# Optimization experiments

Hardware: AMD Instinct MI355X
Metric: run time of the kernel (lower is better)

The kernel has to match this reference:

```python
import jax, jax.numpy as jnp
import numpy as np

NX = 2048
NL = 20
BATCH = 512
EIGMAX = 10.0
EPS = 1e-9


def prox_cardan(eta, x):
    """Prox of u -> -eta*(log(u)+log(1-u)) at x: unique root in (0,1) of
    u^3 - (1+x)u^2 + (x-2eta)u + eta = 0 (Cardano / trigonometric method)."""
    b = -(1.0 + x)
    c = x - 2.0 * eta
    d = eta
    p = c - b * b / 3.0
    q = 2.0 * b ** 3 / 27.0 - b * c / 3.0 + d
    disc = -4.0 * p ** 3 - 27.0 * q ** 2
    # three-real-roots branch (trigonometric); requires p<0
    pm = jnp.minimum(p, -1e-12)
    m = 2.0 * jnp.sqrt(-pm / 3.0)
    arg = jnp.clip(3.0 * q / (pm * m), -1.0, 1.0)
    th = jnp.arccos(arg)
    k = jnp.arange(3, dtype=x.dtype)
    t_trig = m[..., None] * jnp.cos((th[..., None] - 2.0 * jnp.pi * k) / 3.0)
    r_trig = t_trig - b[..., None] / 3.0
    in01 = (r_trig > 0.0) & (r_trig < 1.0)
    idx = jnp.argmax(in01, axis=-1)
    root3 = jnp.take_along_axis(r_trig, idx[..., None], axis=-1)[..., 0]
    # one-real-root branch
    s = jnp.sqrt(jnp.maximum(q * q / 4.0 + p ** 3 / 27.0, 0.0))
    root1 = jnp.cbrt(-q / 2.0 + s) + jnp.cbrt(-q / 2.0 - s) - b / 3.0
    u = jnp.where(disc >= 0.0, root3, root1)
    return jnp.clip(u, EPS, 1.0 - EPS)


def setup_inputs() -> dict:
    key = jax.random.key(0)
    k1, k2, k3, k4, k5 = jax.random.split(key, 5)
    x = jax.random.uniform(k1, (BATCH, 1, NX), dtype=jnp.float32)
    # symmetric PSD operators for T^T T and D^T D (as in a discretized inverse problem)
    A = jax.random.normal(k2, (NX, NX), dtype=jnp.float32)
    tTT = (A @ A.T) / NX
    B = jax.random.normal(k3, (NX, NX), dtype=jnp.float32)
    tDD = (B @ B.T) / NX
    # orthogonal change-of-basis: element <-> eigen bases
    Q, _ = jnp.linalg.qr(jax.random.normal(k4, (NX, NX), dtype=jnp.float32))
    Pelt = Q.astype(jnp.float32)
    Peig = Q.T.astype(jnp.float32)
    x_b = jnp.einsum('ij,bcj->bci', tTT, x) + 0.01 * jax.random.normal(k5, (BATCH, 1, NX), dtype=jnp.float32)
    gamma = jnp.full((NL,), 0.1, dtype=jnp.float32)   # nn.Parameter([0.1])
    mu = jnp.zeros((NL,), dtype=jnp.float32)          # nn.Parameter([0.0])
    reg = jnp.full((NL,), 0.001, dtype=jnp.float32)   # noisy=True -> trainable 0.001
    return {"x": x, "x_b": x_b, "tDD": tDD, "tTT": tTT, "Peig": Peig,
            "Pelt": Pelt, "gamma": gamma, "mu": mu, "reg": reg}


def reference(x, x_b, tDD, tTT, Peig, Pelt, gamma, mu, reg):
    def step(xc, params):
        g_raw, mu_raw, reg_raw = params
        g = jax.nn.softplus(g_raw)
        mu_l = jax.nn.softplus(mu_raw) / 1e6
        reg_l = jax.nn.softplus(reg_raw) / (EIGMAX ** 2)
        grad = (jnp.einsum('ij,bcj->bci', tTT, xc) - x_b
                + reg_l * jnp.einsum('ij,bcj->bci', tDD, xc))
        xt = xc - g * grad
        xt = jnp.einsum('ij,bcj->bci', Pelt, xt)
        xt = prox_cardan(g * mu_l, xt)
        xt = jnp.einsum('ij,bcj->bci', Peig, xt)
        return xt, None

    out, _ = jax.lax.scan(step, x, (gamma, mu, reg))
    return out
```

## Files before the change

kernel.cpp:

```cpp
#include <hip/hip_runtime.h>
#include <math.h>

#define MDIM 512
#define NDIM 2048
#define KDIM 2048
#define NLAYERS 20

static const size_t MN = (size_t)MDIM * NDIM;
static const size_t OPN = (size_t)KDIM * KDIM;

using bf16x8 = __attribute__((ext_vector_type(8))) short;
using f32x4  = __attribute__((ext_vector_type(4))) float;

__device__ __forceinline__ double softplusd(double v) {
    return (v > 20.0) ? v : log1p(exp(v));
}

__device__ __forceinline__ float prox_cardan_f(float eta, float x) {
    const float b  = -(1.0f + x);
    const float c  = x - 2.0f * eta;
    const float dd = eta;
    const float p  = c - b * b * (1.0f / 3.0f);
    const float q  = 2.0f * b * b * b * (1.0f / 27.0f) - b * c * (1.0f / 3.0f) + dd;
    const float disc = -4.0f * p * p * p - 27.0f * q * q;
    const float pm = fminf(p, -1e-12f);
    const float mm = 2.0f * sqrtf(-pm * (1.0f / 3.0f));
    float arg = 3.0f * q / (pm * mm);
    arg = fminf(fmaxf(arg, -1.0f), 1.0f);
    const float th = acosf(arg);
    const float TWO_PI = 6.28318530717958647692f;
    const float r0 = mm * cosf(th * (1.0f / 3.0f)) - b * (1.0f / 3.0f);
    const float r1 = mm * cosf((th - TWO_PI) * (1.0f / 3.0f)) - b * (1.0f / 3.0f);
    const float r2 = mm * cosf((th - 2.0f * TWO_PI) * (1.0f / 3.0f)) - b * (1.0f / 3.0f);
    const bool in0 = (r0 > 0.0f) && (r0 < 1.0f);
    const bool in1 = (r1 > 0.0f) && (r1 < 1.0f);
    const bool in2 = (r2 > 0.0f) && (r2 < 1.0f);
    const float root3 = in0 ? r0 : (in1 ? r1 : (in2 ? r2 : r0));
    const float s = sqrtf(fmaxf(q * q * 0.25f + p * p * p * (1.0f / 27.0f), 0.0f));
    const float root1 = cbrtf(-q * 0.5f + s) + cbrtf(-q * 0.5f - s) - b * (1.0f / 3.0f);
    const float u = (disc >= 0.0f) ? root3 : root1;
    return fminf(fmaxf(u, 1e-9f), 1.0f - 1e-9f);
}

__device__ __forceinline__ double prox_newton_d(double eta, double x) {
    double u = (double)prox_cardan_f((float)eta, (float)x);
#pragma unroll
    for (int i = 0; i < 4; ++i) {
        const double um1 = u - 1.0;
        const double umx = u - x;
        const double P  = u * um1 * umx - eta * (2.0 * u - 1.0);
        const double dP = um1 * umx + u * umx + u * um1 - 2.0 * eta;
        u = u - P / dP;
        u = fmin(fmax(u, 1e-12), 1.0 - 1e-12);
    }
    return fmin(fmax(u, 1e-9), 1.0 - 1e-9);
}

__device__ __forceinline__ unsigned short f2bf(float f) {
    unsigned u = __float_as_uint(f);
    unsigned r = (u + 0x7FFFu + ((u >> 16) & 1u)) >> 16;
    return (unsigned short)r;
}
__device__ __forceinline__ float bf2f(unsigned short h) {
    return __uint_as_float(((unsigned)h) << 16);
}
__device__ __forceinline__ void split3f(float f, unsigned short& b1,
                                        unsigned short& b2, unsigned short& b3) {
    b1 = f2bf(f);
    const float r1 = f - bf2f(b1);
    b2 = f2bf(r1);
    const float r2 = r1 - bf2f(b2);
    b3 = f2bf(r2);
}

__global__ __launch_bounds__(256) void split3_op(
    const float* __restrict__ s1, const float* __restrict__ s2,
    const float* __restrict__ greg, int layer,
    unsigned short* __restrict__ p1, unsigned short* __restrict__ p2,
    unsigned short* __restrict__ p3) {
    const size_t i = ((size_t)blockIdx.x * 256 + threadIdx.x) * 4;
    float reglf = 0.0f;
    if (s2) reglf = (float)(softplusd((double)greg[layer]) * 0.01);
    const float4 a = *(const float4*)(s1 + i);
    float4 b = make_float4(0.f, 0.f, 0.f, 0.f);
    if (s2) b = *(const float4*)(s2 + i);
    ushort4 o1, o2, o3;
    split3f(fmaf(reglf, b.x, a.x), o1.x, o2.x, o3.x);
    split3f(fmaf(reglf, b.y, a.y), o1.y, o2.y, o3.y);
    split3f(fmaf(reglf, b.z, a.z), o1.z, o2.z, o3.z);
    split3f(fmaf(reglf, b.w, a.w), o1.w, o2.w, o3.w);
    *(ushort4*)(p1 + i) = o1;
    *(ushort4*)(p2 + i) = o2;
    *(ushort4*)(p3 + i) = o3;
}

__global__ __launch_bounds__(256) void split3_w(
    const float* __restrict__ s1, const float* __restrict__ s2,
    const float* __restrict__ greg, int layer,
    unsigned short* __restrict__ p1, unsigned short* __restrict__ p2,
    unsigned short* __restrict__ p3) {
    if (layer > 0 && greg[layer] == greg[0]) return;
    const size_t i = ((size_t)blockIdx.x * 256 + threadIdx.x) * 4;
    const float reglf = (float)(softplusd((double)greg[layer]) * 0.01);
    const float4 a = *(const float4*)(s1 + i);
    const float4 b = *(const float4*)(s2 + i);
    ushort4 o1, o2, o3;
    split3f(fmaf(reglf, b.x, a.x), o1.x, o2.x, o3.x);
    split3f(fmaf(reglf, b.y, a.y), o1.y, o2.y, o3.y);
    split3f(fmaf(reglf, b.z, a.z), o1.z, o2.z, o3.z);
    split3f(fmaf(reglf, b.w, a.w), o1.w, o2.w, o3.w);
    *(ushort4*)(p1 + i) = o1;
    *(ushort4*)(p2 + i) = o2;
    *(ushort4*)(p3 + i) = o3;
}

__global__ __launch_bounds__(256, 3) void gemm_bf16x3(
    const unsigned short* __restrict__ A1, const unsigned short* __restrict__ A2,
    const unsigned short* __restrict__ A3,
    const unsigned short* __restrict__ W1, const unsigned short* __restrict__ W2,
    const unsigned short* __restrict__ W3,
    float* __restrict__ Part, int klen) {
    __shared__ __align__(16) unsigned short Ab[3][64][32];
    __shared__ __align__(16) unsigned short Wb[3][64][32];

    const int tid = threadIdx.x;
    const int n0 = blockIdx.x * 64;
    const int m0 = blockIdx.y * 64;
    const int kb = blockIdx.z * klen;
    const int lane = tid & 63, wid = tid >> 6;
    const int quad = lane >> 4, lrow = lane & 15;
    const int wm = (wid >> 1) * 32, wn = (wid & 1) * 32;

    const int srow = tid >> 2;
    const int skc  = (tid & 3) * 8;

    const unsigned short* gA1 = A1 + (size_t)(m0 + srow) * KDIM + kb + skc;
    const unsigned short* gA2 = A2 + (size_t)(m0 + srow) * KDIM + kb + skc;
    const unsigned short* gA3 = A3 + (size_t)(m0 + srow) * KDIM + kb + skc;
    const unsigned short* gW1 = W1 + (size_t)(n0 + srow) * KDIM + kb + skc;
    const unsigned short* gW2 = W2 + (size_t)(n0 + srow) * KDIM + kb + skc;
    const unsigned short* gW3 = W3 + (size_t)(n0 + srow) * KDIM + kb + skc;

    bf16x8 sa1 = *(const bf16x8*)gA1, sa2 = *(const bf16x8*)gA2, sa3 = *(const bf16x8*)gA3;
    bf16x8 sw1 = *(const bf16x8*)gW1, sw2 = *(const bf16x8*)gW2, sw3 = *(const bf16x8*)gW3;

    f32x4 ahi[2][2], alo[2][2];
#pragma unroll
    for (int a = 0; a < 2; ++a)
#pragma unroll
        for (int b = 0; b < 2; ++b) {
            ahi[a][b] = (f32x4){0.f, 0.f, 0.f, 0.f};
            alo[a][b] = (f32x4){0.f, 0.f, 0.f, 0.f};
        }

    for (int k0 = 0; k0 < klen; k0 += 32) {
        *(bf16x8*)&Ab[0][srow][skc] = sa1;
        *(bf16x8*)&Ab[1][srow][skc] = sa2;
        *(bf16x8*)&Ab[2][srow][skc] = sa3;
        *(bf16x8*)&Wb[0][srow][skc] = sw1;
        *(bf16x8*)&Wb[1][srow][skc] = sw2;
        *(bf16x8*)&Wb[2][srow][skc] = sw3;
        __syncthreads();

        if (k0 + 32 < klen) {
            sa1 = *(const bf16x8*)(gA1 + k0 + 32);
            sa2 = *(const bf16x8*)(gA2 + k0 + 32);
            sa3 = *(const bf16x8*)(gA3 + k0 + 32);
            sw1 = *(const bf16x8*)(gW1 + k0 + 32);
            sw2 = *(const bf16x8*)(gW2 + k0 + 32);
            sw3 = *(const bf16x8*)(gW3 + k0 + 32);
        }

        bf16x8 fa[2][3], fw[2][3];
#pragma unroll
        for (int t = 0; t < 2; ++t) {
            const int ra = wm + t * 16 + lrow;
            const int rw = wn + t * 16 + lrow;
            fa[t][0] = *(const bf16x8*)&Ab[0][ra][quad * 8];
            fa[t][1] = *(const bf16x8*)&Ab[1][ra][quad * 8];
            fa[t][2] = *(const bf16x8*)&Ab[2][ra][quad * 8];
            fw[t][0] = *(const bf16x8*)&Wb[0][rw][quad * 8];
            fw[t][1] = *(const bf16x8*)&Wb[1][rw][quad * 8];
            fw[t][2] = *(const bf16x8*)&Wb[2][rw][quad * 8];
        }
#pragma unroll
        for (int tm = 0; tm < 2; ++tm)
#pragma unroll
            for (int tn = 0; tn < 2; ++tn) {
                ahi[tm][tn] = __builtin_amdgcn_mfma_f32_16x16x32_bf16(fa[tm][0], fw[tn][0], ahi[tm][tn], 0, 0, 0);
                alo[tm][tn] = __builtin_amdgcn_mfma_f32_16x16x32_bf16(fa[tm][0], fw[tn][1], alo[tm][tn], 0, 0, 0);
                alo[tm][tn] = __builtin_amdgcn_mfma_f32_16x16x32_bf16(fa[tm][1], fw[tn][0], alo[tm][tn], 0, 0, 0);
                alo[tm][tn] = __builtin_amdgcn_mfma_f32_16x16x32_bf16(fa[tm][1], fw[tn][1], alo[tm][tn], 0, 0, 0);
                alo[tm][tn] = __builtin_amdgcn_mfma_f32_16x16x32_bf16(fa[tm][0], fw[tn][2], alo[tm][tn], 0, 0, 0);
                alo[tm][tn] = __builtin_amdgcn_mfma_f32_16x16x32_bf16(fa[tm][2], fw[tn][0], alo[tm][tn], 0, 0, 0);
            }
        __syncthreads();
    }

    float* P = Part + (size_t)blockIdx.z * MN;
#pragma unroll
    for (int tm = 0; tm < 2; ++tm)
#pragma unroll
        for (int tn = 0; tn < 2; ++tn) {
            const int mbase = m0 + wm + tm * 16 + quad * 4;
            const int nn = n0 + wn + tn * 16 + lrow;
#pragma unroll
            for (int r = 0; r < 4; ++r)
                P[(size_t)(mbase + r) * NDIM + nn] = ahi[tm][tn][r] + alo[tm][tn][r];
        }
}

template <int MODE>
__global__ __launch_bounds__(256) void combine3(
    const float* __restrict__ Part, int S,
    const float* __restrict__ Xc, const float* __restrict__ Xb,
    float* __restrict__ stateOut,
    unsigned short* __restrict__ p1, unsigned short* __restrict__ p2,
    unsigned short* __restrict__ p3,
    const float* __restrict__ gam, const float* __restrict__ gmu,
    const float* __restrict__ greg, int layer) {
    const size_t i = ((size_t)blockIdx.x * 256 + threadIdx.x) * 4;
    double s0 = 0.0, s1 = 0.0, s2 = 0.0, s3 = 0.0;
    for (int z = 0; z < S; ++z) {
        const float4 p = *(const float4*)(Part + (size_t)z * MN + i);
        s0 += (double)p.x; s1 += (double)p.y; s2 += (double)p.z; s3 += (double)p.w;
    }
    float v0, v1, v2, v3;
    if (MODE == 0) {
        const double g = softplusd((double)gam[layer]);
        const float4 xc = *(const float4*)(Xc + i);
        const float4 xb = *(const float4*)(Xb + i);
        v0 = (float)((double)xc.x - g * (s0 - (double)xb.x));
        v1 = (float)((double)xc.y - g * (s1 - (double)xb.y));
        v2 = (float)((double)xc.z - g * (s2 - (double)xb.z));
        v3 = (float)((double)xc.w - g * (s3 - (double)xb.w));
    } else if (MODE == 1) {
        const double g   = softplusd((double)gam[layer]);
        const double eta = g * softplusd((double)gmu[layer]) * 1e-6;
        v0 = (float)prox_newton_d(eta, s0);
        v1 = (float)prox_newton_d(eta, s1);
        v2 = (float)prox_newton_d(eta, s2);
        v3 = (float)prox_newton_d(eta, s3);
    } else {
        v0 = (float)s0; v1 = (float)s1; v2 = (float)s2; v3 = (float)s3;
        *(float4*)(stateOut + i) = make_float4(v0, v1, v2, v3);
    }
    ushort4 o1, o2, o3;
    split3f(v0, o1.x, o2.x, o3.x);
    split3f(v1, o1.y, o2.y, o3.y);
    split3f(v2, o1.z, o2.z, o3.z);
    split3f(v3, o1.w, o2.w, o3.w);
    *(ushort4*)(p1 + i) = o1;
    *(ushort4*)(p2 + i) = o2;
    *(ushort4*)(p3 + i) = o3;
}

#define BM 64
#define BN 64
#define BK 32
#define LDSP 68

__device__ __forceinline__ double prox_cardan_d(double eta, double x) {
    const double b  = -(1.0 + x);
    const double c  = x - 2.0 * eta;
    const double dd = eta;
    const double p  = c - b * b * (1.0 / 3.0);
    const double q  = 2.0 * b * b * b * (1.0 / 27.0) - b * c * (1.0 / 3.0) + dd;
    const double disc = -4.0 * p * p * p - 27.0 * q * q;
    const double pm = fmin(p, -1e-12);
    const double mm = 2.0 * sqrt(-pm * (1.0 / 3.0));
    double arg = 3.0 * q / (pm * mm);
    arg = fmin(fmax(arg, -1.0), 1.0);
    const double th = acos(arg);
    const double TWO_PI = 6.283185307179586476925286766559;
    const double r0 = mm * cos(th * (1.0 / 3.0)) - b * (1.0 / 3.0);
    const double r1 = mm * cos((th - TWO_PI) * (1.0 / 3.0)) - b * (1.0 / 3.0);
    const double r2 = mm * cos((th - 2.0 * TWO_PI) * (1.0 / 3.0)) - b * (1.0 / 3.0);
    const bool in0 = (r0 > 0.0) && (r0 < 1.0);
    const bool in1 = (r1 > 0.0) && (r1 < 1.0);
    const bool in2 = (r2 > 0.0) && (r2 < 1.0);
    const double root3 = in0 ? r0 : (in1 ? r1 : (in2 ? r2 : r0));
    const double s = sqrt(fmax(q * q * 0.25 + p * p * p * (1.0 / 27.0), 0.0));
    const double root1 = cbrt(-q * 0.5 + s) + cbrt(-q * 0.5 - s) - b * (1.0 / 3.0);
    const double u = (disc >= 0.0) ? root3 : root1;
    return fmin(fmax(u, 1e-9), 1.0 - 1e-9);
}

template <bool FUSE2>
__global__ __launch_bounds__(256, 4) void gemm_nt_splitk(
    const float* __restrict__ A, const float* __restrict__ W1,
    const float* __restrict__ W2, double* __restrict__ Part,
    const float* __restrict__ greg, int layer, int klen) {
    __shared__ float As[BK][LDSP];
    __shared__ float Ws[BK][LDSP];
    const int tid = threadIdx.x;
    const int m0 = blockIdx.y * BM;
    const int n0 = blockIdx.x * BN;
    const int kbase = blockIdx.z * klen;
    float reglf = 0.0f;
    if (FUSE2) reglf = (float)(softplusd((double)greg[layer]) * 0.01);
    const int lrow = tid >> 3;
    const int lkc  = (tid & 7) << 2;
    const float* pA  = A  + (size_t)(m0 + lrow) * KDIM + kbase + lkc;
    const float* pW  = W1 + (size_t)(n0 + lrow) * KDIM + kbase + lkc;
    const float* pW2 = FUSE2 ? (W2 + (size_t)(n0 + lrow) * KDIM + kbase + lkc) : nullptr;
    float4 ra[2], rw[2];
    ra[0] = *(const float4*)(pA);
    ra[1] = *(const float4*)(pA + 32 * KDIM);
    rw[0] = *(const float4*)(pW);
    rw[1] = *(const float4*)(pW + 32 * KDIM);
    if (FUSE2) {
        const float4 u0 = *(const float4*)(pW2);
        const float4 u1 = *(const float4*)(pW2 + 32 * KDIM);
        rw[0].x += reglf * u0.x; rw[0].y += reglf * u0.y;
        rw[0].z += reglf * u0.z; rw[0].w += reglf * u0.w;
        rw[1].x += reglf * u1.x; rw[1].y += reglf * u1.y;
        rw[1].z += reglf * u1.z; rw[1].w += reglf * u1.w;
    }
    float  acc[4][4]   = {};
    double acc64[4][4] = {};
    const int tx = (tid & 15) << 2;
    const int ty = (tid >> 4) << 2;
    int it = 0;
    for (int k0 = 0; k0 < klen; k0 += BK, ++it) {
#pragma unroll
        for (int h = 0; h < 2; ++h) {
            const int row = lrow + (h << 5);
            As[lkc + 0][row] = (h ? ra[1].x : ra[0].x);
            As[lkc + 1][row] = (h ? ra[1].y : ra[0].y);
            As[lkc + 2][row] = (h ? ra[1].z : ra[0].z);
            As[lkc + 3][row] = (h ? ra[1].w : ra[0].w);
            Ws[lkc + 0][row] = (h ? rw[1].x : rw[0].x);
            Ws[lkc + 1][row] = (h ? rw[1].y : rw[0].y);
            Ws[lkc + 2][row] = (h ? rw[1].z : rw[0].z);
            Ws[lkc + 3][row] = (h ? rw[1].w : rw[0].w);
        }
        __syncthreads();
        if (k0 + BK < klen) {
            const float* qA = pA + k0 + BK;
            ra[0] = *(const float4*)(qA);
            ra[1] = *(const float4*)(qA + 32 * KDIM);
            const float* qW = pW + k0 + BK;
            rw[0] = *(const float4*)(qW);
            rw[1] = *(const float4*)(qW + 32 * KDIM);
            if (FUSE2) {
                const float* qW2 = pW2 + k0 + BK;
                const float4 u0 = *(const float4*)(qW2);
                const float4 u1 = *(const float4*)(qW2 + 32 * KDIM);
                rw[0].x += reglf * u0.x; rw[0].y += reglf * u0.y;
                rw[0].z += reglf * u0.z; rw[0].w += reglf * u0.w;
                rw[1].x += reglf * u1.x; rw[1].y += reglf * u1.y;
                rw[1].z += reglf * u1.z; rw[1].w += reglf * u1.w;
            }
        }
#pragma unroll
        for (int kk = 0; kk < BK; ++kk) {
            const float4 a4 = *(const float4*)(&As[kk][ty]);
            const float4 b4 = *(const float4*)(&Ws[kk][tx]);
            const float av[4] = {a4.x, a4.y, a4.z, a4.w};
            const float bv[4] = {b4.x, b4.y, b4.z, b4.w};
#pragma unroll
            for (int r = 0; r < 4; ++r)
#pragma unroll
                for (int cc = 0; cc < 4; ++cc)
                    acc[r][cc] = fmaf(av[r], bv[cc], acc[r][cc]);
        }
        __syncthreads();
        if ((it & 1) == 1) {
#pragma unroll
            for (int r = 0; r < 4; ++r)
#pragma unroll
                for (int cc = 0; cc < 4; ++cc) {
                    acc64[r][cc] += (double)acc[r][cc];
                    acc[r][cc] = 0.0f;
                }
        }
    }
#pragma unroll
    for (int r = 0; r < 4; ++r)
#pragma unroll
        for (int cc = 0; cc < 4; ++cc)
            acc64[r][cc] += (double)acc[r][cc];
    double* Pz = Part + (size_t)blockIdx.z * MN;
#pragma unroll
    for (int r = 0; r < 4; ++r) {
        double* q = Pz + (size_t)(m0 + ty + r) * NDIM + n0 + tx;
        *(double2*)(q)     = make_double2(acc64[r][0], acc64[r][1]);
        *(double2*)(q + 2) = make_double2(acc64[r][2], acc64[r][3]);
    }
}

template <int MODE>
__global__ __launch_bounds__(256) void combine_ep(
    const double* __restrict__ Part, int nslices,
    const float* __restrict__ Xc, const float* __restrict__ Xb,
    float* __restrict__ Out,
    const float* __restrict__ gam, const float* __restrict__ gmu,
    const float* __restrict__ greg, int layer) {
    const size_t i4 = ((size_t)blockIdx.x * 256 + threadIdx.x) * 4;
    double s0 = 0.0, s1 = 0.0, s2 = 0.0, s3 = 0.0;
    for (int z = 0; z < nslices; ++z) {
        const double* p = Part + (size_t)z * MN + i4;
        const double2 a = *(const double2*)(p);
        const double2 b = *(const double2*)(p + 2);
        s0 += a.x; s1 += a.y; s2 += b.x; s3 += b.y;
    }
    float4 o;
    if (MODE == 0) {
        const double g = softplusd((double)gam[layer]);
        const float4 xc = *(const float4*)(Xc + i4);
        const float4 xb = *(const float4*)(Xb + i4);
        o.x = (float)((double)xc.x - g * (s0 - (double)xb.x));
        o.y = (float)((double)xc.y - g * (s1 - (double)xb.y));
        o.z = (float)((double)xc.z - g * (s2 - (double)xb.z));
        o.w = (float)((double)xc.w - g * (s3 - (double)xb.w));
    } else if (MODE == 1) {
        const double g   = softplusd((double)gam[layer]);
        const double eta = g * softplusd((double)gmu[layer]) * 1e-6;
        o.x = (float)prox_cardan_d(eta, s0);
        o.y = (float)prox_cardan_d(eta, s1);
        o.z = (float)prox_cardan_d(eta, s2);
        o.w = (float)prox_cardan_d(eta, s3);
    } else {
        o.x = (float)s0; o.y = (float)s1; o.z = (float)s2; o.w = (float)s3;
    }
    *(float4*)(Out + i4) = o;
}

extern "C" void kernel_launch(void* const* d_in, const int* in_sizes, int n_in,
                              void* d_out, int out_size, void* d_ws, size_t ws_size,
                              hipStream_t stream) {
    const float* x    = (const float*)d_in[0];
    const float* x_b  = (const float*)d_in[1];
    const float* tDD  = (const float*)d_in[2];
    const float* tTT  = (const float*)d_in[3];
    const float* Peig = (const float*)d_in[4];
    const float* Pelt = (const float*)d_in[5];
    const float* gam  = (const float*)d_in[6];
    const float* gmu  = (const float*)d_in[7];
    const float* greg = (const float*)d_in[8];
    float* out = (float*)d_out;

    const size_t TRI_OP_B = 3 * OPN * 2;
    const size_t TRI_A_B  = 3 * MN * 2;
    const size_t STATE_B  = MN * 4;
    const size_t full_need = 3 * TRI_OP_B + 2 * TRI_A_B + STATE_B + 2 * MN * 4;
    const size_t mid_need  = 1 * TRI_OP_B + 2 * TRI_A_B + STATE_B + 2 * MN * 4;

    const bool full = (ws_size >= full_need);
    const bool mid  = (!full && ws_size >= mid_need);

    if (full || mid) {
        const int S = 2;
        const int klen = KDIM / S;
        char* p = (char*)d_ws;
        unsigned short *Wt1, *Wt2, *Wt3, *Pe1, *Pe2, *Pe3, *Pg1, *Pg2, *Pg3;
        if (full) {
            Wt1 = (unsigned short*)p;        Wt2 = Wt1 + OPN; Wt3 = Wt2 + OPN; p += TRI_OP_B;
            Pe1 = (unsigned short*)p;        Pe2 = Pe1 + OPN; Pe3 = Pe2 + OPN; p += TRI_OP_B;
            Pg1 = (unsigned short*)p;        Pg2 = Pg1 + OPN; Pg3 = Pg2 + OPN; p += TRI_OP_B;
        } else {
            Wt1 = (unsigned short*)p;        Wt2 = Wt1 + OPN; Wt3 = Wt2 + OPN; p += TRI_OP_B;
            Pe1 = Wt1; Pe2 = Wt2; Pe3 = Wt3;
            Pg1 = Wt1; Pg2 = Wt2; Pg3 = Wt3;
        }
        unsigned short* Aa1 = (unsigned short*)p; unsigned short* Aa2 = Aa1 + MN;
        unsigned short* Aa3 = Aa2 + MN; p += TRI_A_B;
        unsigned short* Ab1 = (unsigned short*)p; unsigned short* Ab2 = Ab1 + MN;
        unsigned short* Ab3 = Ab2 + MN; p += TRI_A_B;
        float* state = (float*)p; p += STATE_B;
        float* part  = (float*)p;

        const dim3 gg(NDIM / 64, MDIM / 64, S);
        const unsigned cgrid = (unsigned)(MN / 4 / 256);
        const unsigned ogrid = (unsigned)(OPN / 4 / 256);

        split3_op<<<cgrid, 256, 0, stream>>>(x, nullptr, greg, 0, Aa1, Aa2, Aa3);
        if (full) {
            split3_op<<<ogrid, 256, 0, stream>>>(Pelt, nullptr, greg, 0, Pe1, Pe2, Pe3);
            split3_op<<<ogrid, 256, 0, stream>>>(Peig, nullptr, greg, 0, Pg1, Pg2, Pg3);
        }

        unsigned short *c1 = Aa1, *c2 = Aa2, *c3 = Aa3;
        unsigned short *d1 = Ab1, *d2 = Ab2, *d3 = Ab3;

        for (int l = 0; l < NLAYERS; ++l) {
            if (full) {
                split3_w<<<ogrid, 256, 0, stream>>>(tTT, tDD, greg, l, Wt1, Wt2, Wt3);
            } else {
                split3_op<<<ogrid, 256, 0, stream>>>(tTT, tDD, greg, l, Wt1, Wt2, Wt3);
            }
            gemm_bf16x3<<<gg, 256, 0, stream>>>(c1, c2, c3, Wt1, Wt2, Wt3, part, klen);
            combine3<0><<<cgrid, 256, 0, stream>>>(part, S, (l == 0 ? x : state), x_b,
                                                   nullptr, d1, d2, d3, gam, gmu, greg, l);
            if (mid) split3_op<<<ogrid, 256, 0, stream>>>(Pelt, nullptr, greg, 0, Pe1, Pe2, Pe3);
            gemm_bf16x3<<<gg, 256, 0, stream>>>(d1, d2, d3, Pe1, Pe2, Pe3, part, klen);
            combine3<1><<<cgrid, 256, 0, stream>>>(part, S, nullptr, nullptr,
                                                   nullptr, c1, c2, c3, gam, gmu, greg, l);
            if (mid) split3_op<<<ogrid, 256, 0, stream>>>(Peig, nullptr, greg, 0, Pg1, Pg2, Pg3);
            gemm_bf16x3<<<gg, 256, 0, stream>>>(c1, c2, c3, Pg1, Pg2, Pg3, part, klen);
            combine3<2><<<cgrid, 256, 0, stream>>>(part, S, nullptr, nullptr,
                                                   (l == NLAYERS - 1 ? out : state),
                                                   d1, d2, d3, gam, gmu, greg, l);
            unsigned short* t;
            t = c1; c1 = d1; d1 = t;
            t = c2; c2 = d2; d2 = t;
            t = c3; c3 = d3; d3 = t;
        }
        return;
    }

    char* wsb = (char*)d_ws;
    float* b0 = (float*)wsb;
    float* b1 = b0 + MN;
    float* b2 = b1 + MN;
    float* b3 = b2 + MN;
    const size_t base_bytes = 4 * MN * sizeof(float);
    double* partd = (double*)(wsb + base_bytes);
    int S = 0;
    if (ws_size >= base_bytes + 2 * MN * sizeof(double)) S = 2;
    else if (ws_size >= base_bytes + 1 * MN * sizeof(double)) S = 1;
    if (S == 0) return;
    const int klen = KDIM / S;
    dim3 gg(NDIM / BN, MDIM / BM, S);
    dim3 cg((unsigned)(MN / 4 / 256));
    const float* cur = x;
    float* bx = b0; float* bu = b1; float* bn = b2; float* bo = b3;
    for (int l = 0; l < NLAYERS; ++l) {
        gemm_nt_splitk<true><<<gg, 256, 0, stream>>>(cur, tTT, tDD, partd, greg, l, klen);
        combine_ep<0><<<cg, 256, 0, stream>>>(partd, S, cur, x_b, bx, gam, gmu, greg, l);
        gemm_nt_splitk<false><<<gg, 256, 0, stream>>>(bx, Pelt, nullptr, partd, greg, l, klen);
        combine_ep<1><<<cg, 256, 0, stream>>>(partd, S, nullptr, nullptr, bu, gam, gmu, greg, l);
        gemm_nt_splitk<false><<<gg, 256, 0, stream>>>(bu, Peig, nullptr, partd, greg, l, klen);
        float* dst = (l == NLAYERS - 1) ? out : bn;
        combine_ep<2><<<cg, 256, 0, stream>>>(partd, S, nullptr, nullptr, dst, gam, gmu, greg, l);
        cur = bn;
        float* t = bn; bn = bo; bo = t;
    }
}
```

Baseline: 2.606 ms.

## Double-buffer GEMM tiles via direct global-to-LDS loads with swizzle and XCD-aware block mapping

The bf16x3 GEMM now loads tiles straight from global memory into LDS with global_load_lds, double-buffers them, and drops one barrier per k-step. An XOR swizzle on the LDS columns avoids bank conflicts on fragment reads. The grid becomes 1-D and is remapped so consecutive blocks on the same XCD share tiles. The aim is to overlap loads with MFMA work and improve L2 locality. The cost is double the LDS use, which may lower occupancy, and a single barrier per iteration that relies on correct ordering of the async LDS writes.

```diff
diff --git a/kernel.cpp b/kernel.cpp
--- a/kernel.cpp
+++ b/kernel.cpp
@@ -73,6 +73,12 @@
     b3 = f2bf(r2);
 }
 
+__device__ __forceinline__ void gl16(const void* g, void* l) {
+    __builtin_amdgcn_global_load_lds(
+        (const __attribute__((address_space(1))) unsigned int*)g,
+        (__attribute__((address_space(3))) unsigned int*)l, 16, 0, 0);
+}
+
 __global__ __launch_bounds__(256) void split3_op(
     const float* __restrict__ s1, const float* __restrict__ s2,
     const float* __restrict__ greg, int layer,
@@ -119,30 +125,42 @@
     const unsigned short* __restrict__ A3,
     const unsigned short* __restrict__ W1, const unsigned short* __restrict__ W2,
     const unsigned short* __restrict__ W3,
-    float* __restrict__ Part, int klen) {
-    __shared__ __align__(16) unsigned short Ab[3][64][32];
-    __shared__ __align__(16) unsigned short Wb[3][64][32];
+    float* __restrict__ Part, int klen, int S) {
+    __shared__ __align__(16) unsigned short Ab[2][3][64][32];
+    __shared__ __align__(16) unsigned short Wb[2][3][64][32];
 
     const int tid = threadIdx.x;
-    const int n0 = blockIdx.x * 64;
-    const int m0 = blockIdx.y * 64;
-    const int kb = blockIdx.z * klen;
+
+    const int nwg = 256 * S;
+    const int cpx = nwg >> 3;
+    const int bid = blockIdx.x;
+    const int g   = (bid & 7) * cpx + (bid >> 3);
+    const int xs  = g / (8 * S);
+    const int rr  = g - xs * (8 * S);
+    const int ys  = rr & 7;
+    const int zs  = rr >> 3;
+    const int n0 = xs * 64;
+    const int m0 = ys * 64;
+    const int kb = zs * klen;
+
     const int lane = tid & 63, wid = tid >> 6;
     const int quad = lane >> 4, lrow = lane & 15;
     const int wm = (wid >> 1) * 32, wn = (wid & 1) * 32;
 
     const int srow = tid >> 2;
-    const int skc  = (tid & 3) * 8;
-
-    const unsigned short* gA1 = A1 + (size_t)(m0 + srow) * KDIM + kb + skc;
-    const unsigned short* gA2 = A2 + (size_t)(m0 + srow) * KDIM + kb + skc;
-    const unsigned short* gA3 = A3 + (size_t)(m0 + srow) * KDIM + kb + skc;
-    const unsigned short* gW1 = W1 + (size_t)(n0 + srow) * KDIM + kb + skc;
-    const unsigned short* gW2 = W2 + (size_t)(n0 + srow) * KDIM + kb + skc;
-    const unsigned short* gW3 = W3 + (size_t)(n0 + srow) * KDIM + kb + skc;
-
-    bf16x8 sa1 = *(const bf16x8*)gA1, sa2 = *(const bf16x8*)gA2, sa3 = *(const bf16x8*)gA3;
-    bf16x8 sw1 = *(const bf16x8*)gW1, sw2 = *(const bf16x8*)gW2, sw3 = *(const bf16x8*)gW3;
+    const int lc8  = ((tid & 3) ^ ((tid >> 3) & 3)) * 8;
+    const int t8   = tid * 8;
+    const int qx   = (quad ^ ((lrow >> 1) & 3)) * 8;
+
+    const unsigned short* gA1 = A1 + (size_t)(m0 + srow) * KDIM + kb + lc8;
+    const unsigned short* gA2 = A2 + (size_t)(m0 + srow) * KDIM + kb + lc8;
+    const unsigned short* gA3 = A3 + (size_t)(m0 + srow) * KDIM + kb + lc8;
+    const unsigned short* gW1 = W1 + (size_t)(n0 + srow) * KDIM + kb + lc8;
+    const unsigned short* gW2 = W2 + (size_t)(n0 + srow) * KDIM + kb + lc8;
+    const unsigned short* gW3 = W3 + (size_t)(n0 + srow) * KDIM + kb + lc8;
+
+    unsigned short* lA = &Ab[0][0][0][0];
+    unsigned short* lW = &Wb[0][0][0][0];
 
     f32x4 ahi[2][2], alo[2][2];
 #pragma unroll
@@ -153,35 +171,41 @@
             alo[a][b] = (f32x4){0.f, 0.f, 0.f, 0.f};
         }
 
+    gl16(gA1, lA + t8);
+    gl16(gA2, lA + 2048 + t8);
+    gl16(gA3, lA + 4096 + t8);
+    gl16(gW1, lW + t8);
+    gl16(gW2, lW + 2048 + t8);
+    gl16(gW3, lW + 4096 + t8);
+
+    int cur = 0;
     for (int k0 = 0; k0 < klen; k0 += 32) {
-        *(bf16x8*)&Ab[0][srow][skc] = sa1;
-        *(bf16x8*)&Ab[1][srow][skc] = sa2;
-        *(bf16x8*)&Ab[2][srow][skc] = sa3;
-        *(bf16x8*)&Wb[0][srow][skc] = sw1;
-        *(bf16x8*)&Wb[1][srow][skc] = sw2;
-        *(bf16x8*)&Wb[2][srow][skc] = sw3;
         __syncthreads();
 
         if (k0 + 32 < klen) {
-            sa1 = *(const bf16x8*)(gA1 + k0 + 32);
-            sa2 = *(const bf16x8*)(gA2 + k0 + 32);
-            sa3 = *(const bf16x8*)(gA3 + k0 + 32);
-            sw1 = *(const bf16x8*)(gW1 + k0 + 32);
-            sw2 = *(const bf16x8*)(gW2 + k0 + 32);
-            sw3 = *(const bf16x8*)(gW3 + k0 + 32);
-        }
+            const int nb = (cur ^ 1) * 6144;
+            gl16(gA1 + k0 + 32, lA + nb + t8);
+            gl16(gA2 + k0 + 32, lA + nb + 2048 + t8);
+            gl16(gA3 + k0 + 32, lA + nb + 4096 + t8);
+            gl16(gW1 + k0 + 32, lW + nb + t8);
+            gl16(gW2 + k0 + 32, lW + nb + 2048 + t8);
+            gl16(gW3 + k0 + 32, lW + nb + 4096 + t8);
+        }
+
+        const unsigned short* cA = lA + cur * 6144;
+        const unsigned short* cW = lW + cur * 6144;
 
         bf16x8 fa[2][3], fw[2][3];
 #pragma unroll
         for (int t = 0; t < 2; ++t) {
-            const int ra = wm + t * 16 + lrow;
-            const int rw = wn + t * 16 + lrow;
-            fa[t][0] = *(const bf16x8*)&Ab[0][ra][quad * 8];
-            fa[t][1] = *(const bf16x8*)&Ab[1][ra][quad * 8];
-            fa[t][2] = *(const bf16x8*)&Ab[2][ra][quad * 8];
-            fw[t][0] = *(const bf16x8*)&Wb[0][rw][quad * 8];
-            fw[t][1] = *(const bf16x8*)&Wb[1][rw][quad * 8];
-            fw[t][2] = *(const bf16x8*)&Wb[2][rw][quad * 8];
+            const int ra = (wm + t * 16 + lrow) * 32;
+            const int rw = (wn + t * 16 + lrow) * 32;
+            fa[t][0] = *(const bf16x8*)(cA + ra + qx);
+            fa[t][1] = *(const bf16x8*)(cA + 2048 + ra + qx);
+            fa[t][2] = *(const bf16x8*)(cA + 4096 + ra + qx);
+            fw[t][0] = *(const bf16x8*)(cW + rw + qx);
+            fw[t][1] = *(const bf16x8*)(cW + 2048 + rw + qx);
+            fw[t][2] = *(const bf16x8*)(cW + 4096 + rw + qx);
         }
 #pragma unroll
         for (int tm = 0; tm < 2; ++tm)
@@ -194,10 +218,10 @@
                 alo[tm][tn] = __builtin_amdgcn_mfma_f32_16x16x32_bf16(fa[tm][0], fw[tn][2], alo[tm][tn], 0, 0, 0);
                 alo[tm][tn] = __builtin_amdgcn_mfma_f32_16x16x32_bf16(fa[tm][2], fw[tn][0], alo[tm][tn], 0, 0, 0);
             }
-        __syncthreads();
-    }
-
-    float* P = Part + (size_t)blockIdx.z * MN;
+        cur ^= 1;
+    }
+
+    float* P = Part + (size_t)zs * MN;
 #pragma unroll
     for (int tm = 0; tm < 2; ++tm)
 #pragma unroll
@@ -471,7 +495,7 @@
         float* state = (float*)p; p += STATE_B;
         float* part  = (float*)p;
 
-        const dim3 gg(NDIM / 64, MDIM / 64, S);
+        const dim3 gg((unsigned)(256 * S));
         const unsigned cgrid = (unsigned)(MN / 4 / 256);
         const unsigned ogrid = (unsigned)(OPN / 4 / 256);
 
@@ -490,15 +514,15 @@
             } else {
                 split3_op<<<ogrid, 256, 0, stream>>>(tTT, tDD, greg, l, Wt1, Wt2, Wt3);
             }
-            gemm_bf16x3<<<gg, 256, 0, stream>>>(c1, c2, c3, Wt1, Wt2, Wt3, part, klen);
+            gemm_bf16x3<<<gg, 256, 0, stream>>>(c1, c2, c3, Wt1, Wt2, Wt3, part, klen, S);
             combine3<0><<<cgrid, 256, 0, stream>>>(part, S, (l == 0 ? x : state), x_b,
                                                    nullptr, d1, d2, d3, gam, gmu, greg, l);
             if (mid) split3_op<<<ogrid, 256, 0, stream>>>(Pelt, nullptr, greg, 0, Pe1, Pe2, Pe3);
-            gemm_bf16x3<<<gg, 256, 0, stream>>>(d1, d2, d3, Pe1, Pe2, Pe3, part, klen);
+            gemm_bf16x3<<<gg, 256, 0, stream>>>(d1, d2, d3, Pe1, Pe2, Pe3, part, klen, S);
             combine3<1><<<cgrid, 256, 0, stream>>>(part, S, nullptr, nullptr,
                                                    nullptr, c1, c2, c3, gam, gmu, greg, l);
             if (mid) split3_op<<<ogrid, 256, 0, stream>>>(Peig, nullptr, greg, 0, Pg1, Pg2, Pg3);
-            gemm_bf16x3<<<gg, 256, 0, stream>>>(c1, c2, c3, Pg1, Pg2, Pg3, part, klen);
+            gemm_bf16x3<<<gg, 256, 0, stream>>>(c1, c2, c3, Pg1, Pg2, Pg3, part, klen, S);
             combine3<2><<<cgrid, 256, 0, stream>>>(part, S, nullptr, nullptr,
                                                    (l == NLAYERS - 1 ? out : state),
                                                    d1, d2, d3, gam, gmu, greg, l);
```

Result: no change. 2.620 ms (+0.5%).

## Rewrite bf16x3 GEMM as single-wave 32x32 tiles loading directly from global

Applied to the files above, without the earlier changes.

The split-bf16 GEMM moves from 256-thread 64x64 tiles staged through LDS to single-wavefront 32x32 tiles whose MFMA fragments are loaded straight from global memory, with register double-buffering and raised wave priority around the MFMA blocks. The launch becomes a 1D grid remapped with an XCD-style swizzle (bid&7) so neighbouring tiles share caches. The goal is to remove LDS round-trips and block barriers and to put more independent waves in flight. In exchange, each tile gets less operand reuse, so more data comes from global memory and L2, and the global loads are strided 16-byte row fragments.

```diff
diff --git a/kernel.cpp b/kernel.cpp
--- a/kernel.cpp
+++ b/kernel.cpp
@@ -114,35 +114,38 @@
     *(ushort4*)(p3 + i) = o3;
 }
 
-__global__ __launch_bounds__(256, 3) void gemm_bf16x3(
+__global__ __launch_bounds__(64, 2) void gemm_bf16x3(
     const unsigned short* __restrict__ A1, const unsigned short* __restrict__ A2,
     const unsigned short* __restrict__ A3,
     const unsigned short* __restrict__ W1, const unsigned short* __restrict__ W2,
     const unsigned short* __restrict__ W3,
-    float* __restrict__ Part, int klen) {
-    __shared__ __align__(16) unsigned short Ab[3][64][32];
-    __shared__ __align__(16) unsigned short Wb[3][64][32];
-
-    const int tid = threadIdx.x;
-    const int n0 = blockIdx.x * 64;
-    const int m0 = blockIdx.y * 64;
-    const int kb = blockIdx.z * klen;
-    const int lane = tid & 63, wid = tid >> 6;
+    float* __restrict__ Part, int klen, int S) {
+    const int lane = threadIdx.x;
+
+    const int nwg = (NDIM / 32) * (MDIM / 32) * S;
+    const int cpx = nwg >> 3;
+    const int bid = blockIdx.x;
+    const int g   = (bid & 7) * cpx + (bid >> 3);
+    const int per_x = (MDIM / 32) * S;
+    const int xs  = g / per_x;
+    const int rr  = g - xs * per_x;
+    const int ys  = rr & (MDIM / 32 - 1);
+    const int zs  = rr >> 4;
+    const int n0 = xs * 32;
+    const int m0 = ys * 32;
+    const int kb = zs * klen;
+
     const int quad = lane >> 4, lrow = lane & 15;
-    const int wm = (wid >> 1) * 32, wn = (wid & 1) * 32;
-
-    const int srow = tid >> 2;
-    const int skc  = (tid & 3) * 8;
-
-    const unsigned short* gA1 = A1 + (size_t)(m0 + srow) * KDIM + kb + skc;
-    const unsigned short* gA2 = A2 + (size_t)(m0 + srow) * KDIM + kb + skc;
-    const unsigned short* gA3 = A3 + (size_t)(m0 + srow) * KDIM + kb + skc;
-    const unsigned short* gW1 = W1 + (size_t)(n0 + srow) * KDIM + kb + skc;
-    const unsigned short* gW2 = W2 + (size_t)(n0 + srow) * KDIM + kb + skc;
-    const unsigned short* gW3 = W3 + (size_t)(n0 + srow) * KDIM + kb + skc;
-
-    bf16x8 sa1 = *(const bf16x8*)gA1, sa2 = *(const bf16x8*)gA2, sa3 = *(const bf16x8*)gA3;
-    bf16x8 sw1 = *(const bf16x8*)gW1, sw2 = *(const bf16x8*)gW2, sw3 = *(const bf16x8*)gW3;
+
+    const unsigned short* pa[2][3];
+    const unsigned short* pw[2][3];
+#pragma unroll
+    for (int t = 0; t < 2; ++t) {
+        const size_t ra = (size_t)(m0 + t * 16 + lrow) * KDIM + kb + quad * 8;
+        const size_t rw = (size_t)(n0 + t * 16 + lrow) * KDIM + kb + quad * 8;
+        pa[t][0] = A1 + ra; pa[t][1] = A2 + ra; pa[t][2] = A3 + ra;
+        pw[t][0] = W1 + rw; pw[t][1] = W2 + rw; pw[t][2] = W3 + rw;
+    }
 
     f32x4 ahi[2][2], alo[2][2];
 #pragma unroll
@@ -153,36 +156,18 @@
             alo[a][b] = (f32x4){0.f, 0.f, 0.f, 0.f};
         }
 
-    for (int k0 = 0; k0 < klen; k0 += 32) {
-        *(bf16x8*)&Ab[0][srow][skc] = sa1;
-        *(bf16x8*)&Ab[1][srow][skc] = sa2;
-        *(bf16x8*)&Ab[2][srow][skc] = sa3;
-        *(bf16x8*)&Wb[0][srow][skc] = sw1;
-        *(bf16x8*)&Wb[1][srow][skc] = sw2;
-        *(bf16x8*)&Wb[2][srow][skc] = sw3;
-        __syncthreads();
-
-        if (k0 + 32 < klen) {
-            sa1 = *(const bf16x8*)(gA1 + k0 + 32);
-            sa2 = *(const bf16x8*)(gA2 + k0 + 32);
-            sa3 = *(const bf16x8*)(gA3 + k0 + 32);
-            sw1 = *(const bf16x8*)(gW1 + k0 + 32);
-            sw2 = *(const bf16x8*)(gW2 + k0 + 32);
-            sw3 = *(const bf16x8*)(gW3 + k0 + 32);
-        }
-
-        bf16x8 fa[2][3], fw[2][3];
+    auto LOAD = [&](bf16x8 (&fa)[2][3], bf16x8 (&fw)[2][3], int k0) {
 #pragma unroll
         for (int t = 0; t < 2; ++t) {
-            const int ra = wm + t * 16 + lrow;
-            const int rw = wn + t * 16 + lrow;
-            fa[t][0] = *(const bf16x8*)&Ab[0][ra][quad * 8];
-            fa[t][1] = *(const bf16x8*)&Ab[1][ra][quad * 8];
-            fa[t][2] = *(const bf16x8*)&Ab[2][ra][quad * 8];
-            fw[t][0] = *(const bf16x8*)&Wb[0][rw][quad * 8];
-            fw[t][1] = *(const bf16x8*)&Wb[1][rw][quad * 8];
-            fw[t][2] = *(const bf16x8*)&Wb[2][rw][quad * 8];
-        }
+#pragma unroll
+            for (int p = 0; p < 3; ++p) {
+                fa[t][p] = *(const bf16x8*)(pa[t][p] + k0);
+                fw[t][p] = *(const bf16x8*)(pw[t][p] + k0);
+            }
+        }
+    };
+    auto MF = [&](bf16x8 (&fa)[2][3], bf16x8 (&fw)[2][3]) {
+        __builtin_amdgcn_s_setprio(1);
 #pragma unroll
         for (int tm = 0; tm < 2; ++tm)
 #pragma unroll
@@ -194,16 +179,29 @@
                 alo[tm][tn] = __builtin_amdgcn_mfma_f32_16x16x32_bf16(fa[tm][0], fw[tn][2], alo[tm][tn], 0, 0, 0);
                 alo[tm][tn] = __builtin_amdgcn_mfma_f32_16x16x32_bf16(fa[tm][2], fw[tn][0], alo[tm][tn], 0, 0, 0);
             }
-        __syncthreads();
-    }
-
-    float* P = Part + (size_t)blockIdx.z * MN;
+        __builtin_amdgcn_s_setprio(0);
+    };
+
+    const int nsteps = klen >> 5;
+
+    bf16x8 fa0[2][3], fw0[2][3], fa1[2][3], fw1[2][3];
+    LOAD(fa0, fw0, 0);
+    for (int s = 0; s < nsteps; s += 2) {
+        if (s + 1 < nsteps) LOAD(fa1, fw1, (s + 1) * 32);
+        MF(fa0, fw0);
+        if (s + 1 < nsteps) {
+            if (s + 2 < nsteps) LOAD(fa0, fw0, (s + 2) * 32);
+            MF(fa1, fw1);
+        }
+    }
+
+    float* P = Part + (size_t)zs * MN;
 #pragma unroll
     for (int tm = 0; tm < 2; ++tm)
 #pragma unroll
         for (int tn = 0; tn < 2; ++tn) {
-            const int mbase = m0 + wm + tm * 16 + quad * 4;
-            const int nn = n0 + wn + tn * 16 + lrow;
+            const int mbase = m0 + tm * 16 + quad * 4;
+            const int nn = n0 + tn * 16 + lrow;
 #pragma unroll
             for (int r = 0; r < 4; ++r)
                 P[(size_t)(mbase + r) * NDIM + nn] = ahi[tm][tn][r] + alo[tm][tn][r];
@@ -471,7 +469,7 @@
         float* state = (float*)p; p += STATE_B;
         float* part  = (float*)p;
 
-        const dim3 gg(NDIM / 64, MDIM / 64, S);
+        const dim3 gg((unsigned)((NDIM / 32) * (MDIM / 32) * S));
         const unsigned cgrid = (unsigned)(MN / 4 / 256);
         const unsigned ogrid = (unsigned)(OPN / 4 / 256);
 
@@ -490,15 +488,15 @@
             } else {
                 split3_op<<<ogrid, 256, 0, stream>>>(tTT, tDD, greg, l, Wt1, Wt2, Wt3);
             }
-            gemm_bf16x3<<<gg, 256, 0, stream>>>(c1, c2, c3, Wt1, Wt2, Wt3, part, klen);
+            gemm_bf16x3<<<gg, 64, 0, stream>>>(c1, c2, c3, Wt1, Wt2, Wt3, part, klen, S);
             combine3<0><<<cgrid, 256, 0, stream>>>(part, S, (l == 0 ? x : state), x_b,
                                                    nullptr, d1, d2, d3, gam, gmu, greg, l);
             if (mid) split3_op<<<ogrid, 256, 0, stream>>>(Pelt, nullptr, greg, 0, Pe1, Pe2, Pe3);
-            gemm_bf16x3<<<gg, 256, 0, stream>>>(d1, d2, d3, Pe1, Pe2, Pe3, part, klen);
+            gemm_bf16x3<<<gg, 64, 0, stream>>>(d1, d2, d3, Pe1, Pe2, Pe3, part, klen, S);
             combine3<1><<<cgrid, 256, 0, stream>>>(part, S, nullptr, nullptr,
                                                    nullptr, c1, c2, c3, gam, gmu, greg, l);
             if (mid) split3_op<<<ogrid, 256, 0, stream>>>(Peig, nullptr, greg, 0, Pg1, Pg2, Pg3);
-            gemm_bf16x3<<<gg, 256, 0, stream>>>(c1, c2, c3, Pg1, Pg2, Pg3, part, klen);
+            gemm_bf16x3<<<gg, 64, 0, stream>>>(c1, c2, c3, Pg1, Pg2, Pg3, part, klen, S);
             combine3<2><<<cgrid, 256, 0, stream>>>(part, S, nullptr, nullptr,
                                                    (l == NLAYERS - 1 ? out : state),
                                                    d1, d2, d3, gam, gmu, greg, l);
```

After: 5.899 ms. +126.3%, slower.
